# Kernel optimization log

Measured on AMD Instinct MI355X. Metric: run time of the kernel, lower is better.

## Reference

```python
import jax, jax.numpy as jnp
import numpy as np

P = 10          # num_patches
EPS = 1e-20
ALPHAS = dict(stretch=1.0, E=1.0, G=1.0, skew=1.0, total_area=1.0, total_area_mult=1.0)
ALPHA_MC = 1.0
ALPHA_DISTORT = 1.0


def setup_inputs() -> dict:
    key = jax.random.key(0)
    k1, k2, k3, k4 = jax.random.split(key, 4)
    B, N, M = 8, 8192, 2500
    pc_gt = jax.random.normal(k1, (B, N, 3), dtype=jnp.float32)
    pc_pred = jax.random.normal(k2, (B, M, 3), dtype=jnp.float32)
    # first fundamental form (E, F, G); ensure E*G - F^2 > 0 so sqrt is smooth
    u = jax.random.uniform(k3, (B, M, 3), dtype=jnp.float32)
    fff = u * 0.5 + jnp.array([1.0, 0.0, 1.0], dtype=jnp.float32)
    A_gt = jax.random.uniform(k4, (B,), dtype=jnp.float32)
    return {"pc_gt": pc_gt, "pc_pred": pc_pred, "fff": fff, "A_gt": A_gt}


def _forward(pc_gt, pc_pred, fff, A_gt):
    B, M, _ = pc_pred.shape
    spp = M // P

    # ---- Chamfer distance via dense (B, M, N) distance matrix + argmin ----
    diff = pc_pred[:, :, None, :] - pc_gt[:, None, :, :]          # (B, M, N, 3)
    distm = jnp.sqrt(jnp.sum(diff * diff, axis=3))                # (B, M, N)
    inds_p2gt = jnp.argmin(distm, axis=2)                         # (B, M)
    inds_gt2p = jnp.argmin(distm, axis=1)                         # (B, N)
    pc_gt_reg = jnp.take_along_axis(pc_gt, inds_p2gt[..., None], axis=1)   # (B, M, 3)
    pc_p_reg = jnp.take_along_axis(pc_pred, inds_gt2p[..., None], axis=1)  # (B, N, 3)
    d_p2gt = jnp.sum((pc_pred - pc_gt_reg) ** 2, axis=2)
    d_gt2p = jnp.sum((pc_gt - pc_p_reg) ** 2, axis=2)
    L_chd = d_p2gt.mean() + d_gt2p.mean()

    # ---- FFF-based losses ----
    EFG = jnp.transpose(fff.reshape(B, P, spp, 3), (3, 0, 1, 2))  # (3, B, P, spp)
    E, F, G = EFG[0], EFG[1], EFG[2]

    # metric consistency between consecutive frame pairs
    Eh = E.reshape(B // 2, 2, P, spp)
    Fh = F.reshape(B // 2, 2, P, spp)
    Gh = G.reshape(B // 2, 2, P, spp)
    L_mc = ((Eh[:, 0] - Eh[:, 1]) ** 2
            + 2.0 * (Fh[:, 0] - Fh[:, 1]) ** 2
            + (Gh[:, 0] - Gh[:, 1]) ** 2).mean()

    # scaled isometry (collapse) losses
    A2 = jnp.maximum(E * G - F * F, 0.0)                          # (B, P, spp)
    A = jnp.sqrt(A2)
    inv = 1.0 / (A2 + EPS)
    L_stretch = (((E - G) ** 2) * inv).mean() * ALPHAS['stretch']
    L_E = (((E - E.mean()) ** 2) * inv).mean() * ALPHAS['E']
    L_G = (((G - G.mean()) ** 2) * inv).mean() * ALPHAS['G']
    L_F = ((F * F) * inv).mean() * ALPHAS['skew']

    # overlap / total-area loss
    A_tot = A.mean(axis=2).sum(axis=1)                            # (B,)
    L_olap = (jnp.maximum(0.0, A_tot - A_gt * ALPHAS['total_area_mult']) ** 2).mean() * ALPHAS['total_area']

    loss_sciso = L_F + L_E + L_G + L_stretch + L_olap
    loss_tot = L_chd + ALPHA_MC * L_mc + ALPHA_DISTORT * loss_sciso
    return loss_tot


def reference(pc_gt, pc_pred, fff, A_gt):
    return _forward(pc_gt, pc_pred, fff, A_gt)
```

## Files before the change

kernel.cpp:

```cpp
#include <hip/hip_runtime.h>

#define B_   8
#define N_   8192
#define M_   2500
#define SPP_ 250
#define EPS_ 1e-20f
#define BIGF 1e30f

#define NB_P2GT 320
#define NB_GT2P 256
#define NB_FFF  79
#define NB_K1   (NB_P2GT + NB_GT2P + NB_FFF)

#define NB_RG2P 64
#define NB_RP2  20
#define NB_K2   (NB_RG2P + NB_RP2)

#define WS_P2GT 0
#define WS_GT2P 160000
#define WS_F1P  291072
#define WS_RED  292968
#define WS_CNT  293052
#define RO_G2P 0
#define RO_P2  64
#define F_E    0
#define F_G    1
#define F_MC   2
#define F_ST   3
#define F_F2I  4
#define F_E2I  5
#define F_EI   6
#define F_G2I  7
#define F_GI   8
#define F_I    9
#define F_AB   10

typedef __attribute__((ext_vector_type(8))) short short8_t;
typedef __attribute__((ext_vector_type(4))) float float4_t;

__device__ __forceinline__ unsigned pack_bf2(float lo, float hi) {
    unsigned a = __float_as_uint(lo);
    unsigned b = __float_as_uint(hi);
    a = (a + 0x7FFFu + ((a >> 16) & 1u)) >> 16;
    b = (b + 0x7FFFu + ((b >> 16) & 1u)) & 0xFFFF0000u;
    return a | b;
}
__device__ __forceinline__ short bf16s(float x) {
    unsigned a = __float_as_uint(x);
    return (short)((a + 0x7FFFu + ((a >> 16) & 1u)) >> 16);
}
__device__ __forceinline__ float wave_sum64(float v) {
    #pragma unroll
    for (int o = 32; o > 0; o >>= 1) v += __shfl_down(v, o, 64);
    return v;
}
__device__ __forceinline__ float block_sum256(float v, volatile float* red4) {
    v = wave_sum64(v);
    int wid = threadIdx.x >> 6, lane = threadIdx.x & 63;
    if (lane == 0) red4[wid] = v;
    __syncthreads();
    float r = 0.f;
    if (threadIdx.x == 0) r = red4[0] + red4[1] + red4[2] + red4[3];
    __syncthreads();
    return r;
}
__device__ __forceinline__ void min4(float4_t& c, const float4_t d) {
    c.x = fminf(c.x, d.x); c.y = fminf(c.y, d.y);
    c.z = fminf(c.z, d.z); c.w = fminf(c.w, d.w);
}
__device__ __forceinline__ void quad_min4(float4_t& c) {
    #pragma unroll
    for (int m = 1; m < 16; m <<= 1) {
        c.x = fminf(c.x, __shfl_xor(c.x, m, 64));
        c.y = fminf(c.y, __shfl_xor(c.y, m, 64));
        c.z = fminf(c.z, __shfl_xor(c.z, m, 64));
        c.w = fminf(c.w, __shfl_xor(c.w, m, 64));
    }
}

__global__ void __launch_bounds__(256, 2) k1_main(
        const float* __restrict__ gt, const float* __restrict__ pred,
        const float* __restrict__ fff, float* __restrict__ ws) {
    __shared__ uint4 spts[1280];
    __shared__ __align__(16) float saux[520];
    const int bid = blockIdx.x;
    const int tid = threadIdx.x;
    const int lane = tid & 63;
    const int w    = tid >> 6;
    const int quad = lane >> 4;
    const int l15  = lane & 15;

    if (bid == 0 && tid == 0) ((unsigned*)(ws + WS_CNT))[0] = 0u;

    if (bid < NB_P2GT + NB_GT2P) {
        const bool is_p2gt = bid < NB_P2GT;
        int b, mblk, z, ntiles, blim, alim;
        const float* apts; const float* bpts; float* dst;
        if (is_p2gt) {
            z = bid / 40; int rem = bid % 40;
            b = rem / 5;  mblk = rem % 5;
            apts = pred + (size_t)b * M_ * 3;
            bpts = gt + ((size_t)b * N_ + (size_t)z * 1024) * 3;
            ntiles = 64; blim = 1024; alim = M_;
            dst = ws + WS_P2GT + (size_t)z * 20000 + b * M_;
        } else {
            int r = bid - NB_P2GT;
            z = r >> 7; int rem = r & 127;
            b = rem >> 4; mblk = rem & 15;
            apts = gt + (size_t)b * N_ * 3;
            bpts = pred + ((size_t)b * M_ + (size_t)z * 1280) * 3;
            ntiles = 80; blim = M_ - z * 1280; alim = N_;
            dst = ws + WS_GT2P + (size_t)z * 65536 + b * N_;
        }
        const int abase = mblk * 512;
        const int nstage = ntiles * 16;

        for (int i = tid; i < nstage; i += 256) {
            float x = 0.f, y = 0.f, zc = 0.f, n2 = BIGF;
            if (i < blim) {
                x = bpts[i * 3 + 0]; y = bpts[i * 3 + 1]; zc = bpts[i * 3 + 2];
                n2 = x * x + y * y + zc * zc;
            }
            uint4 q;
            q.x = pack_bf2(-2.f * x, -2.f * y);
            q.y = pack_bf2(-2.f * zc, n2);
            q.z = q.x; q.w = q.y;
            spts[i] = q;
        }

        short8_t af[8];
        #pragma unroll
        for (int t = 0; t < 8; ++t) af[t] = (short8_t){0,0,0,0,0,0,0,0};
        if (lane < 16) {
            #pragma unroll
            for (int t = 0; t < 8; ++t) {
                int m = abase + w * 128 + t * 16 + l15;
                int c = m < alim ? m : alim - 1;
                float x = apts[c*3+0], y = apts[c*3+1], zc = apts[c*3+2];
                af[t][0] = bf16s(x); af[t][1] = bf16s(y); af[t][2] = bf16s(zc);
                af[t][3] = (short)0x3F80;
                saux[w * 128 + t * 16 + l15] = x*x + y*y + zc*zc;
            }
        }
        __syncthreads();

        const float4_t* bp = (const float4_t*)saux;
        float4_t bias[8], c[8];
        #pragma unroll
        for (int t = 0; t < 8; ++t) {
            bias[t] = bp[w * 32 + t * 4 + quad];
            c[t] = (float4_t){BIGF, BIGF, BIGF, BIGF};
        }

        const uint4* bptr = spts + l15;
        #pragma unroll 2
        for (int i = 0; i < ntiles; ++i) {
            short8_t bf = __builtin_bit_cast(short8_t, bptr[i * 16]);
            #pragma unroll
            for (int t = 0; t < 8; ++t) {
                float4_t d = __builtin_amdgcn_mfma_f32_16x16x32_bf16(
                                 af[t], bf, bias[t], 0, 0, 0);
                min4(c[t], d);
            }
        }
        #pragma unroll
        for (int t = 0; t < 8; ++t) {
            quad_min4(c[t]);
            c[t].x = fmaxf(c[t].x, 0.f); c[t].y = fmaxf(c[t].y, 0.f);
            c[t].z = fmaxf(c[t].z, 0.f); c[t].w = fmaxf(c[t].w, 0.f);
        }
        if (l15 == 0) {
            #pragma unroll
            for (int t = 0; t < 8; ++t) {
                int m0 = abase + w * 128 + t * 16 + quad * 4;
                if (m0 < alim)
                    *(float4_t*)(dst + m0) = c[t];
            }
        }
    } else {
        const int kb = bid - NB_P2GT - NB_GT2P;
        const int i  = kb * 256 + tid;
        volatile float* red4 = saux + 512;
        float* sA = saux;
        if (tid < B_) sA[tid] = 0.f;
        __syncthreads();

        float vE=0.f,vG=0.f,vMC=0.f,vST=0.f,vF2=0.f,vE2=0.f,vEI=0.f,
              vG2=0.f,vGI=0.f,vI=0.f;
        if (i < B_ * M_) {
            const int b = i / M_;
            const int m = i - b * M_;
            const float* f = fff + (size_t)i * 3;
            float E = f[0], F = f[1], G = f[2];
            float A2  = fmaxf(E * G - F * F, 0.f);
            float inv = 1.f / (A2 + EPS_);
            vE = E; vG = G;
            vST = (E - G) * (E - G) * inv;
            vF2 = F * F * inv;
            vE2 = E * E * inv; vEI = E * inv;
            vG2 = G * G * inv; vGI = G * inv;
            vI  = inv;
            atomicAdd(&sA[b], sqrtf(A2));
            if ((b & 1) == 0) {
                const float* f2 = fff + ((size_t)(b + 1) * M_ + m) * 3;
                float dE = E - f2[0], dF = F - f2[1], dG = G - f2[2];
                vMC = dE * dE + 2.f * dF * dF + dG * dG;
            }
        }
        float* outp = ws + WS_F1P + (size_t)kb * 24;
        float r;
        r = block_sum256(vE,  red4); if (tid==0) outp[F_E]   = r;
        r = block_sum256(vG,  red4); if (tid==0) outp[F_G]   = r;
        r = block_sum256(vMC, red4); if (tid==0) outp[F_MC]  = r;
        r = block_sum256(vST, red4); if (tid==0) outp[F_ST]  = r;
        r = block_sum256(vF2, red4); if (tid==0) outp[F_F2I] = r;
        r = block_sum256(vE2, red4); if (tid==0) outp[F_E2I] = r;
        r = block_sum256(vEI, red4); if (tid==0) outp[F_EI]  = r;
        r = block_sum256(vG2, red4); if (tid==0) outp[F_G2I] = r;
        r = block_sum256(vGI, red4); if (tid==0) outp[F_GI]  = r;
        r = block_sum256(vI,  red4); if (tid==0) outp[F_I]   = r;
        __syncthreads();
        if (tid < B_) outp[F_AB + tid] = sA[tid];
    }
}

__global__ void __launch_bounds__(256) k2_reduce(
        const float* __restrict__ fff, const float* __restrict__ A_gt,
        float* __restrict__ ws, float* __restrict__ out) {
    __shared__ float red4[4];
    const int bid = blockIdx.x;
    const int tid = threadIdx.x;
    float* redp = ws + WS_RED;
    const float* f1p = ws + WS_F1P;

    if (bid < NB_RG2P) {
        const int o = bid * 1024 + tid * 4;
        const float4_t v0 = *(const float4_t*)(ws + WS_GT2P + o);
        const float4_t v1 = *(const float4_t*)(ws + WS_GT2P + 65536 + o);
        float s = fminf(v0.x, v1.x) + fminf(v0.y, v1.y)
                + fminf(v0.z, v1.z) + fminf(v0.w, v1.w);
        float r = block_sum256(s, red4);
        if (tid == 0) redp[RO_G2P + bid] = r;
    } else {
        const int kb = bid - NB_RG2P;
        const int o = kb * 1024 + tid * 4;
        float s = 0.f;
        if (o < 20000) {
            const float* src = ws + WS_P2GT + o;
            float4_t m = *(const float4_t*)src;
            #pragma unroll
            for (int zz = 1; zz < 8; ++zz) {
                float4_t v = *(const float4_t*)(src + zz * 20000);
                m.x = fminf(m.x, v.x); m.y = fminf(m.y, v.y);
                m.z = fminf(m.z, v.z); m.w = fminf(m.w, v.w);
            }
            s = m.x + m.y + m.z + m.w;
        }
        float r = block_sum256(s, red4);
        if (tid == 0) redp[RO_P2 + kb] = r;
    }

    __syncthreads();
    if (tid == 0) __threadfence();
    __syncthreads();
    __shared__ unsigned old_s;
    if (tid == 0)
        old_s = __hip_atomic_fetch_add((unsigned*)(ws + WS_CNT), 1u,
                                       __ATOMIC_ACQ_REL, __HIP_MEMORY_SCOPE_AGENT);
    __syncthreads();
    if (old_s == (unsigned)(NB_K2 - 1)) {
        float v;
        v = (tid < NB_RG2P) ? redp[RO_G2P + tid] : 0.f;
        float sGT2P = block_sum256(v, red4);
        v = (tid < NB_RP2) ? redp[RO_P2 + tid] : 0.f;
        float sP2GT = block_sum256(v, red4);
        float a[18];
        #pragma unroll
        for (int k = 0; k < 18; ++k) {
            v = (tid < 79) ? f1p[tid * 24 + k] : 0.f;
            a[k] = block_sum256(v, red4);
        }
        if (tid == 0) {
            const float inv20k = 1.f / 20000.f;
            float mE = a[F_E] * inv20k, mG = a[F_G] * inv20k;
            float L_E = (a[F_E2I] - 2.f*mE*a[F_EI] + mE*mE*a[F_I]) * inv20k;
            float L_G = (a[F_G2I] - 2.f*mG*a[F_GI] + mG*mG*a[F_I]) * inv20k;
            float L_sc = L_E + L_G + (a[F_ST] + a[F_F2I]) * inv20k;
            float L_mc = a[F_MC] * (1.f / 10000.f);
            float L_chd = sP2GT * inv20k + sGT2P * (1.f / 65536.f);
            float L_olap = 0.f;
            #pragma unroll
            for (int b = 0; b < B_; ++b) {
                float At = a[F_AB + b] * (1.f / (float)SPP_);
                float d  = fmaxf(0.f, At - A_gt[b]);
                L_olap += d * d;
            }
            L_olap *= (1.f / (float)B_);
            out[0] = L_chd + L_mc + L_sc + L_olap;
        }
    }
}

extern "C" void kernel_launch(void* const* d_in, const int* in_sizes, int n_in,
                              void* d_out, int out_size, void* d_ws, size_t ws_size,
                              hipStream_t stream) {
    const float* pc_gt   = (const float*)d_in[0];
    const float* pc_pred = (const float*)d_in[1];
    const float* fff     = (const float*)d_in[2];
    const float* A_gt    = (const float*)d_in[3];
    float* ws  = (float*)d_ws;
    float* out = (float*)d_out;

    k1_main  <<<NB_K1, 256, 0, stream>>>(pc_gt, pc_pred, fff, ws);
    k2_reduce<<<NB_K2, 256, 0, stream>>>(fff, A_gt, ws, out);
}
```

Before: 97.47 us.

## Switch Chamfer distance MFMA from 16x16x32 to 32x32x16 with norm folded into K

The pairwise distance tiles now use 32x32x16 bf16 MFMA instead of 16x16x32, so each instruction covers 32 points on each side and the per-tile loop runs half as many iterations. The squared norm of the A points is packed into the K dimension as an extra bf16 term, replacing the fp32 bias accumulator that was read from shared memory. This removes the saux bias staging and halves the MFMA count per point pair. In exchange the A norm is now rounded to bf16, which adds error to the distances, and the final cross-lane min reduction needs 5 shuffle steps over 16 values per tile.

Result: slower. 102.4 us (+5.0%).

```diff
diff --git a/kernel.cpp b/kernel.cpp
--- a/kernel.cpp
+++ b/kernel.cpp
@@ -35,8 +35,9 @@
 #define F_I    9
 #define F_AB   10
 
-typedef __attribute__((ext_vector_type(8))) short short8_t;
-typedef __attribute__((ext_vector_type(4))) float float4_t;
+typedef __attribute__((ext_vector_type(8)))  short short8_t;
+typedef __attribute__((ext_vector_type(4)))  float float4_t;
+typedef __attribute__((ext_vector_type(16))) float float16_t;
 
 __device__ __forceinline__ unsigned pack_bf2(float lo, float hi) {
     unsigned a = __float_as_uint(lo);
@@ -64,31 +65,19 @@
     __syncthreads();
     return r;
 }
-__device__ __forceinline__ void min4(float4_t& c, const float4_t d) {
-    c.x = fminf(c.x, d.x); c.y = fminf(c.y, d.y);
-    c.z = fminf(c.z, d.z); c.w = fminf(c.w, d.w);
-}
-__device__ __forceinline__ void quad_min4(float4_t& c) {
-    #pragma unroll
-    for (int m = 1; m < 16; m <<= 1) {
-        c.x = fminf(c.x, __shfl_xor(c.x, m, 64));
-        c.y = fminf(c.y, __shfl_xor(c.y, m, 64));
-        c.z = fminf(c.z, __shfl_xor(c.z, m, 64));
-        c.w = fminf(c.w, __shfl_xor(c.w, m, 64));
-    }
-}
 
 __global__ void __launch_bounds__(256, 2) k1_main(
         const float* __restrict__ gt, const float* __restrict__ pred,
         const float* __restrict__ fff, float* __restrict__ ws) {
     __shared__ uint4 spts[1280];
-    __shared__ __align__(16) float saux[520];
+    __shared__ __align__(16) float saux[8];
+    __shared__ float sA[B_];
     const int bid = blockIdx.x;
     const int tid = threadIdx.x;
     const int lane = tid & 63;
     const int w    = tid >> 6;
-    const int quad = lane >> 4;
-    const int l15  = lane & 15;
+    const int l31  = lane & 31;
+    const int half = lane >> 5;
 
     if (bid == 0 && tid == 0) ((unsigned*)(ws + WS_CNT))[0] = 0u;
 
@@ -101,7 +90,7 @@
             b = rem / 5;  mblk = rem % 5;
             apts = pred + (size_t)b * M_ * 3;
             bpts = gt + ((size_t)b * N_ + (size_t)z * 1024) * 3;
-            ntiles = 64; blim = 1024; alim = M_;
+            ntiles = 32; blim = 1024; alim = M_;
             dst = ws + WS_P2GT + (size_t)z * 20000 + b * M_;
         } else {
             int r = bid - NB_P2GT;
@@ -109,11 +98,11 @@
             b = rem >> 4; mblk = rem & 15;
             apts = gt + (size_t)b * N_ * 3;
             bpts = pred + ((size_t)b * M_ + (size_t)z * 1280) * 3;
-            ntiles = 80; blim = M_ - z * 1280; alim = N_;
+            ntiles = 40; blim = M_ - z * 1280; alim = N_;
             dst = ws + WS_GT2P + (size_t)z * 65536 + b * N_;
         }
         const int abase = mblk * 512;
-        const int nstage = ntiles * 16;
+        const int nstage = ntiles * 32;
 
         for (int i = tid; i < nstage; i += 256) {
             float x = 0.f, y = 0.f, zc = 0.f, n2 = BIGF;
@@ -124,64 +113,77 @@
             uint4 q;
             q.x = pack_bf2(-2.f * x, -2.f * y);
             q.y = pack_bf2(-2.f * zc, n2);
-            q.z = q.x; q.w = q.y;
+            q.z = 0x00003F80u;
+            q.w = 0u;
             spts[i] = q;
         }
 
-        short8_t af[8];
+        short8_t af[4];
         #pragma unroll
-        for (int t = 0; t < 8; ++t) af[t] = (short8_t){0,0,0,0,0,0,0,0};
-        if (lane < 16) {
-            #pragma unroll
-            for (int t = 0; t < 8; ++t) {
-                int m = abase + w * 128 + t * 16 + l15;
+        for (int t = 0; t < 4; ++t) af[t] = (short8_t){0,0,0,0,0,0,0,0};
+        if (half == 0) {
+            #pragma unroll
+            for (int t = 0; t < 4; ++t) {
+                int m = abase + w * 128 + t * 32 + l31;
                 int c = m < alim ? m : alim - 1;
                 float x = apts[c*3+0], y = apts[c*3+1], zc = apts[c*3+2];
+                float n2 = x*x + y*y + zc*zc;
                 af[t][0] = bf16s(x); af[t][1] = bf16s(y); af[t][2] = bf16s(zc);
                 af[t][3] = (short)0x3F80;
-                saux[w * 128 + t * 16 + l15] = x*x + y*y + zc*zc;
+                af[t][4] = bf16s(n2);
             }
         }
         __syncthreads();
 
-        const float4_t* bp = (const float4_t*)saux;
-        float4_t bias[8], c[8];
+        const float16_t z16 = (float16_t)0.f;
+        float16_t c[4];
         #pragma unroll
-        for (int t = 0; t < 8; ++t) {
-            bias[t] = bp[w * 32 + t * 4 + quad];
-            c[t] = (float4_t){BIGF, BIGF, BIGF, BIGF};
-        }
-
-        const uint4* bptr = spts + l15;
+        for (int t = 0; t < 4; ++t) c[t] = (float16_t)BIGF;
+
+        const uint4* bptr = spts + l31;
         #pragma unroll 2
         for (int i = 0; i < ntiles; ++i) {
-            short8_t bf = __builtin_bit_cast(short8_t, bptr[i * 16]);
-            #pragma unroll
-            for (int t = 0; t < 8; ++t) {
-                float4_t d = __builtin_amdgcn_mfma_f32_16x16x32_bf16(
-                                 af[t], bf, bias[t], 0, 0, 0);
-                min4(c[t], d);
-            }
-        }
+            short8_t bf = __builtin_bit_cast(short8_t, bptr[i * 32]);
+            #pragma unroll
+            for (int t = 0; t < 4; ++t) {
+                float16_t d = __builtin_amdgcn_mfma_f32_32x32x16_bf16(
+                                  af[t], bf, z16, 0, 0, 0);
+                #pragma unroll
+                for (int r = 0; r < 16; ++r) c[t][r] = fminf(c[t][r], d[r]);
+            }
+        }
+
         #pragma unroll
-        for (int t = 0; t < 8; ++t) {
-            quad_min4(c[t]);
-            c[t].x = fmaxf(c[t].x, 0.f); c[t].y = fmaxf(c[t].y, 0.f);
-            c[t].z = fmaxf(c[t].z, 0.f); c[t].w = fmaxf(c[t].w, 0.f);
-        }
-        if (l15 == 0) {
-            #pragma unroll
-            for (int t = 0; t < 8; ++t) {
-                int m0 = abase + w * 128 + t * 16 + quad * 4;
-                if (m0 < alim)
-                    *(float4_t*)(dst + m0) = c[t];
+        for (int t = 0; t < 4; ++t) {
+            #pragma unroll
+            for (int m = 1; m < 32; m <<= 1) {
+                #pragma unroll
+                for (int r = 0; r < 16; ++r)
+                    c[t][r] = fminf(c[t][r], __shfl_xor(c[t][r], m, 64));
+            }
+        }
+        if (l31 == 0) {
+            #pragma unroll
+            for (int t = 0; t < 4; ++t) {
+                int tb = abase + w * 128 + t * 32 + 4 * half;
+                #pragma unroll
+                for (int j = 0; j < 4; ++j) {
+                    int m0 = tb + 8 * j;
+                    if (m0 < alim) {
+                        float4_t v;
+                        v.x = fmaxf(c[t][4*j+0], 0.f);
+                        v.y = fmaxf(c[t][4*j+1], 0.f);
+                        v.z = fmaxf(c[t][4*j+2], 0.f);
+                        v.w = fmaxf(c[t][4*j+3], 0.f);
+                        *(float4_t*)(dst + m0) = v;
+                    }
+                }
             }
         }
     } else {
         const int kb = bid - NB_P2GT - NB_GT2P;
         const int i  = kb * 256 + tid;
-        volatile float* red4 = saux + 512;
-        float* sA = saux;
+        volatile float* red4 = saux;
         if (tid < B_) sA[tid] = 0.f;
         __syncthreads();
 
```
